# Performance work log

Hardware: AMD Instinct MI355X
Metric: run time of the kernel (lower is better)

## Reference

```python
import jax, jax.numpy as jnp
import numpy as np

B, NGT, G, C = 2, 64, 6, 64
NVOX = 100000            # occupied voxels per batch element
STRIDE = 4               # x_conv3 stride
RADIUS = 0.4             # pool radius (meters)
PCR = (0.0, -40.0, -3.0)
VOX = (0.05, 0.05, 0.1)
DZ, DY, DX = 10, 400, 352  # downsampled sparse grid (z, y, x)


def setup_inputs() -> dict:
    key = jax.random.key(0)
    k = jax.random.split(key, 10)
    cx = jax.random.uniform(k[0], (B, NGT, 1), minval=5.0, maxval=65.0)
    cy = jax.random.uniform(k[1], (B, NGT, 1), minval=-35.0, maxval=35.0)
    cz = jax.random.uniform(k[2], (B, NGT, 1), minval=-1.5, maxval=0.5)
    dims = jax.random.uniform(k[3], (B, NGT, 3), minval=1.5, maxval=4.5)
    heading = jax.random.uniform(k[4], (B, NGT, 1), minval=-np.pi, maxval=np.pi)
    label = jax.random.randint(k[5], (B, NGT, 1), 1, 4).astype(jnp.float32)
    gt_boxes = jnp.concatenate([cx, cy, cz, dims, heading, label], -1)

    def make_voxels(kc, kf):
        kz, ky, kx = jax.random.split(kc, 3)
        z = jax.random.randint(kz, (B * NVOX,), 0, DZ)
        y = jax.random.randint(ky, (B * NVOX,), 0, DY)
        x = jax.random.randint(kx, (B * NVOX,), 0, DX)
        b = jnp.repeat(jnp.arange(B), NVOX)
        coords = jnp.stack([b, z, y, x], 1).astype(jnp.int32)  # (N, 4) bzyx
        feats = jax.random.normal(kf, (B * NVOX, C), dtype=jnp.float32)
        return coords, feats

    cd, fd = make_voxels(k[6], k[7])
    cs, fs = make_voxels(k[8], k[9])
    return {"gt_boxes": gt_boxes,
            "voxel_coords_dir": cd, "voxel_feats_dir": fd,
            "voxel_coords_dsr": cs, "voxel_feats_dsr": fs}


def _grid_points(gt_boxes):
    # get_dense_grid_points + rotate_points_along_z + global shift
    rois = gt_boxes.reshape(-1, gt_boxes.shape[-1])  # (R, 8)
    g = jnp.arange(G, dtype=jnp.float32)
    idx = jnp.stack(jnp.meshgrid(g, g, g, indexing='ij'), -1).reshape(-1, 3)  # (G^3, 3)
    size = rois[:, 3:6]
    local = (idx[None] + 0.5) / G * size[:, None] - size[:, None] * 0.5  # (R, G^3, 3)
    h = rois[:, 6]
    c, s = jnp.cos(h)[:, None], jnp.sin(h)[:, None]
    x, y, z = local[..., 0], local[..., 1], local[..., 2]
    rot = jnp.stack([x * c - y * s, x * s + y * c, z], -1)
    return rot + rois[:, None, 0:3]  # (R, G^3, 3) global grid points


def _pool(grid_xyz, grid_zyx, gbatch, coords, feats):
    # voxel2pinds hash table: (B, DZ, DY, DX) -> point index or -1
    Ntot = coords.shape[0]
    v2p = jnp.full((B, DZ, DY, DX), -1, jnp.int32)
    v2p = v2p.at[coords[:, 0], coords[:, 1], coords[:, 2], coords[:, 3]].set(
        jnp.arange(Ntot, dtype=jnp.int32))
    # voxel centers (get_voxel_centers with downsample=STRIDE)
    vsz = jnp.array([VOX[0] * STRIDE, VOX[1] * STRIDE, VOX[2] * STRIDE], jnp.float32)
    vox_xyz = (coords[:, jnp.array([3, 2, 1])].astype(jnp.float32) + 0.5) * vsz + jnp.array(PCR, jnp.float32)
    # 3x3x3 neighbor window (QUERY_RANGES = [1,1,1])
    o = jnp.arange(-1, 2)
    offs = jnp.stack(jnp.meshgrid(o, o, o, indexing='ij'), -1).reshape(-1, 3)  # (27, 3) zyx
    nb = grid_zyx[:, None, :] + offs[None]  # (M, 27, 3)
    dims = jnp.array([DZ, DY, DX])
    inb = jnp.all((nb >= 0) & (nb < dims), -1)
    nbc = jnp.clip(nb, 0, dims - 1)
    flat = ((gbatch[:, None] * DZ + nbc[..., 0]) * DY + nbc[..., 1]) * DX + nbc[..., 2]
    pidx = v2p.reshape(-1)[flat]  # (M, 27)
    valid = inb & (pidx >= 0)
    psafe = jnp.where(valid, pidx, 0)
    nxyz = vox_xyz[psafe]  # (M, 27, 3)
    d2 = jnp.sum((nxyz - grid_xyz[:, None]) ** 2, -1)
    m = (valid & (d2 < RADIUS * RADIUS)).astype(feats.dtype)  # ball-query mask
    nf = feats[psafe]  # (M, 27, C) irregular gather
    return jnp.einsum('mkc,mk->mc', nf, m) / jnp.maximum(m.sum(-1), 1.0)[:, None]


def _forward(gt_boxes, voxel_coords_dir, voxel_feats_dir, voxel_coords_dsr, voxel_feats_dsr):
    grid = _grid_points(gt_boxes)            # (R, G^3, 3)
    grid_xyz = grid.reshape(-1, 3)           # (M, 3)
    cf = jnp.floor((grid_xyz - jnp.array(PCR, jnp.float32)) / jnp.array(VOX, jnp.float32))
    cds = jnp.floor(cf / STRIDE).astype(jnp.int32)  # xyz coords at stride
    grid_zyx = cds[:, ::-1]
    R = gt_boxes.shape[0] * gt_boxes.shape[1]
    gbatch = jnp.repeat(jnp.arange(B), NGT * G ** 3)

    def branch(coords, feats):
        p = _pool(grid_xyz, grid_zyx, gbatch, coords, feats)  # (M, C)
        gfeat = p.reshape(R, G ** 3, C).mean(1)               # avg_pool1d over grid pts
        n = jnp.sqrt(jnp.sum(gfeat ** 2, -1, keepdims=True))
        return gfeat / jnp.maximum(n, 1e-12)                  # F.normalize(dim=1)

    fdir = branch(voxel_coords_dir, voxel_feats_dir)
    fdsr = branch(voxel_coords_dsr, voxel_feats_dsr)
    return jnp.mean(jnp.abs(jnp.sum(fdir * fdsr, -1)))


def reference(gt_boxes, voxel_coords_dir, voxel_feats_dir, voxel_coords_dsr, voxel_feats_dsr):
    return _forward(gt_boxes, voxel_coords_dir, voxel_feats_dir, voxel_coords_dsr, voxel_feats_dsr)
```

## Files before the change

### kernel.cpp

```cpp
#include <hip/hip_runtime.h>

#define B_     2
#define NGT_   64
#define G_     6
#define C_     64
#define NVOX_  100000
#define DZ_    10
#define DY_    400
#define DX_    352
#define NPTS   (B_ * NVOX_)
#define NROI   (B_ * NGT_)
#define NGP    (G_ * G_ * G_)
#define M_     (NROI * NGP)
#define VCELLS (B_ * DZ_ * DY_ * DX_)

#define WPB    8
#define JPR    (NGP / WPB)
#define SCAT_BLOCKS ((2 * NPTS + 255) / 256)
#define POOL_BLOCKS (2 * M_ / WPB)

__global__ __launch_bounds__(256) void scatter_kernel(
    const int* __restrict__ cdir, const int* __restrict__ cdsr,
    int* __restrict__ v2p) {
  int i = blockIdx.x * 256 + threadIdx.x;
  if (i >= 2 * NPTS) return;
  int br = (i >= NPTS) ? 1 : 0;
  int p  = i - br * NPTS;
  const int* cb = br ? cdsr : cdir;
  int4 v = ((const int4*)cb)[p];
  int flat = ((v.x * DZ_ + v.y) * DY_ + v.z) * DX_ + v.w;
  atomicMax(&v2p[(long long)br * VCELLS + flat], p);
}

__global__ __launch_bounds__(512) void pool_kernel(
    const float* __restrict__ gt,
    const float* __restrict__ fdir, const float* __restrict__ fdsr,
    const int* __restrict__ v2p, float* __restrict__ part) {
#pragma clang fp contract(off)
  __shared__ float red[WPB][C_];
  int wid  = threadIdx.x >> 6;
  int lane = threadIdx.x & 63;
  int w    = blockIdx.x * WPB + wid;
  int br   = (w >= M_) ? 1 : 0;
  int rem  = w - br * M_;
  int roi  = rem / NGP;
  int gp   = rem - roi * NGP;

  const float* fb  = br ? fdsr : fdir;
  const int*   vpb = v2p + (long long)br * VCELLS;

  const float* r8 = gt + roi * 8;
  float cx = r8[0], cy = r8[1], cz = r8[2];
  float d0 = r8[3], d1 = r8[4], d2s = r8[5];
  float h  = r8[6];

  int ii = gp / 36, jj = (gp / 6) % 6, kk = gp % 6;
  float tx = (ii + 0.5f) / 6.0f;
  float ty = (jj + 0.5f) / 6.0f;
  float tz = (kk + 0.5f) / 6.0f;
  float lx = tx * d0 - d0 * 0.5f;
  float ly = ty * d1 - d1 * 0.5f;
  float lz = tz * d2s - d2s * 0.5f;
  float ch = cosf(h), sh = sinf(h);
  float gx = (lx * ch - ly * sh) + cx;
  float gy = (lx * sh + ly * ch) + cy;
  float gz = lz + cz;

  float fx = floorf((gx - 0.0f)   / 0.05f);
  float fy = floorf((gy + 40.0f)  / 0.05f);
  float fz = floorf((gz + 3.0f)   / 0.1f);
  int ixc = (int)floorf(fx * 0.25f);
  int iyc = (int)floorf(fy * 0.25f);
  int izc = (int)floorf(fz * 0.25f);

  int b = roi >> 6;

  int  pidx_l = -1;
  bool valid  = false;
  if (lane < 27) {
    int oz = lane / 9 - 1, oy = (lane / 3) % 3 - 1, ox = lane % 3 - 1;
    int nz = izc + oz, ny = iyc + oy, nx = ixc + ox;
    if (nz >= 0 && nz < DZ_ && ny >= 0 && ny < DY_ && nx >= 0 && nx < DX_) {
      float vx = ((float)nx + 0.5f) * 0.2f + 0.0f;
      float vy = ((float)ny + 0.5f) * 0.2f + (-40.0f);
      float vz = ((float)nz + 0.5f) * 0.4f + (-3.0f);
      float ddx = vx - gx, ddy = vy - gy, ddz = vz - gz;
      float dd = (ddx * ddx + ddy * ddy) + ddz * ddz;
      if (dd < 0.16f) {
        int flat = ((b * DZ_ + nz) * DY_ + ny) * DX_ + nx;
        int p = vpb[flat];
        if (p >= 0) { valid = true; pidx_l = p; }
      }
    }
  }

  unsigned long long ball = __ballot(valid);
  int cnt = __popcll(ball);
  float acc = 0.0f;
  unsigned long long mm = ball;
  while (mm) {
    int k = (int)__builtin_ctzll(mm);
    mm &= mm - 1;
    int p = __shfl(pidx_l, k, 64);
    acc += fb[(long long)p * C_ + lane];
  }
  float pooled = acc / fmaxf((float)cnt, 1.0f);

  red[wid][lane] = pooled;
  __syncthreads();
  if (wid == 0) {
    float s = 0.0f;
#pragma unroll
    for (int q = 0; q < WPB; ++q) s += red[q][lane];
    part[(long long)blockIdx.x * C_ + lane] = s;
  }
}

__global__ __launch_bounds__(64) void reduce_kernel(
    const float* __restrict__ part, float* __restrict__ gsum) {
  int t = threadIdx.x;
  const float* p = part + (long long)blockIdx.x * JPR * C_;
  float s = 0.0f;
#pragma unroll
  for (int j = 0; j < JPR; ++j) s += p[j * C_ + t];
  gsum[blockIdx.x * C_ + t] = s;
}

__global__ __launch_bounds__(1024) void final_kernel(
    const float* __restrict__ gsum, float* __restrict__ out) {
  __shared__ float partsm[16];
  int wave = threadIdx.x >> 6, lane = threadIdx.x & 63;
  float acc = 0.0f;
  for (int r = wave; r < NROI; r += 16) {
    float a = gsum[r * C_ + lane];
    float b = gsum[(NROI + r) * C_ + lane];
    float dot = a * b, na = a * a, nb = b * b;
    for (int off = 32; off; off >>= 1) {
      dot += __shfl_xor(dot, off, 64);
      na  += __shfl_xor(na,  off, 64);
      nb  += __shfl_xor(nb,  off, 64);
    }
    acc += fabsf(dot) / (fmaxf(sqrtf(na), 1e-12f) * fmaxf(sqrtf(nb), 1e-12f));
  }
  if (lane == 0) partsm[wave] = acc;
  __syncthreads();
  if (threadIdx.x == 0) {
    float s = 0.0f;
    for (int i = 0; i < 16; ++i) s += partsm[i];
    out[0] = s / 128.0f;
  }
}

extern "C" void kernel_launch(void* const* d_in, const int* in_sizes, int n_in,
                              void* d_out, int out_size, void* d_ws, size_t ws_size,
                              hipStream_t stream) {
  const float* gt   = (const float*)d_in[0];
  const int*   cdir = (const int*)d_in[1];
  const float* fdir = (const float*)d_in[2];
  const int*   cdsr = (const int*)d_in[3];
  const float* fdsr = (const float*)d_in[4];
  float* out = (float*)d_out;

  int*   v2p  = (int*)d_ws;
  float* part = (float*)((char*)d_ws + (size_t)2 * VCELLS * 4);
  float* gsum = part + (size_t)POOL_BLOCKS * C_;

  scatter_kernel<<<SCAT_BLOCKS, 256, 0, stream>>>(cdir, cdsr, v2p);
  pool_kernel<<<POOL_BLOCKS, 512, 0, stream>>>(gt, fdir, fdsr, v2p, part);
  reduce_kernel<<<256, 64, 0, stream>>>(part, gsum);
  final_kernel<<<1, 1024, 0, stream>>>(gsum, out);
}
```

Measured before the change: 167.9 us.

## Batch four feature gathers per iteration and fuse reduce with final kernel

The pooling loop now extracts up to four neighbor indices before issuing their feature loads, so several independent global loads can be in flight at once instead of one serialized load per iteration. The separate reduce and single-block final kernels are merged into one per-ROI kernel that reduces both branches, computes the normalized dot term and atomically adds it into the output, which is zeroed in the scatter kernel. This removes one kernel launch and the serial single-block tail, at the cost of a non-deterministic float atomic summation order.

```diff
diff --git a/kernel.cpp b/kernel.cpp
--- a/kernel.cpp
+++ b/kernel.cpp
@@ -21,8 +21,9 @@
 
 __global__ __launch_bounds__(256) void scatter_kernel(
     const int* __restrict__ cdir, const int* __restrict__ cdsr,
-    int* __restrict__ v2p) {
+    int* __restrict__ v2p, float* __restrict__ out) {
   int i = blockIdx.x * 256 + threadIdx.x;
+  if (i == 0) out[0] = 0.0f;
   if (i >= 2 * NPTS) return;
   int br = (i >= NPTS) ? 1 : 0;
   int p  = i - br * NPTS;
@@ -99,10 +100,19 @@
   float acc = 0.0f;
   unsigned long long mm = ball;
   while (mm) {
-    int k = (int)__builtin_ctzll(mm);
-    mm &= mm - 1;
-    int p = __shfl(pidx_l, k, 64);
-    acc += fb[(long long)p * C_ + lane];
+    int p0, p1 = -1, p2 = -1, p3 = -1;
+    { int k = (int)__builtin_ctzll(mm); mm &= mm - 1; p0 = __shfl(pidx_l, k, 64); }
+    if (mm) { int k = (int)__builtin_ctzll(mm); mm &= mm - 1; p1 = __shfl(pidx_l, k, 64); }
+    if (mm) { int k = (int)__builtin_ctzll(mm); mm &= mm - 1; p2 = __shfl(pidx_l, k, 64); }
+    if (mm) { int k = (int)__builtin_ctzll(mm); mm &= mm - 1; p3 = __shfl(pidx_l, k, 64); }
+    float v0 = fb[(long long)p0 * C_ + lane];
+    float v1 = (p1 >= 0) ? fb[(long long)p1 * C_ + lane] : 0.0f;
+    float v2 = (p2 >= 0) ? fb[(long long)p2 * C_ + lane] : 0.0f;
+    float v3 = (p3 >= 0) ? fb[(long long)p3 * C_ + lane] : 0.0f;
+    acc += v0;
+    if (p1 >= 0) acc += v1;
+    if (p2 >= 0) acc += v2;
+    if (p3 >= 0) acc += v3;
   }
   float pooled = acc / fmaxf((float)cnt, 1.0f);
 
@@ -116,38 +126,26 @@
   }
 }
 
-__global__ __launch_bounds__(64) void reduce_kernel(
-    const float* __restrict__ part, float* __restrict__ gsum) {
+__global__ __launch_bounds__(64) void reduce_final_kernel(
+    const float* __restrict__ part, float* __restrict__ out) {
   int t = threadIdx.x;
-  const float* p = part + (long long)blockIdx.x * JPR * C_;
-  float s = 0.0f;
+  int r = blockIdx.x;
+  const float* pa = part + (long long)r * JPR * C_;
+  const float* pb = part + (long long)(NROI * JPR + r * JPR) * C_;
+  float a = 0.0f, b = 0.0f;
 #pragma unroll
-  for (int j = 0; j < JPR; ++j) s += p[j * C_ + t];
-  gsum[blockIdx.x * C_ + t] = s;
-}
-
-__global__ __launch_bounds__(1024) void final_kernel(
-    const float* __restrict__ gsum, float* __restrict__ out) {
-  __shared__ float partsm[16];
-  int wave = threadIdx.x >> 6, lane = threadIdx.x & 63;
-  float acc = 0.0f;
-  for (int r = wave; r < NROI; r += 16) {
-    float a = gsum[r * C_ + lane];
-    float b = gsum[(NROI + r) * C_ + lane];
-    float dot = a * b, na = a * a, nb = b * b;
-    for (int off = 32; off; off >>= 1) {
-      dot += __shfl_xor(dot, off, 64);
-      na  += __shfl_xor(na,  off, 64);
-      nb  += __shfl_xor(nb,  off, 64);
-    }
-    acc += fabsf(dot) / (fmaxf(sqrtf(na), 1e-12f) * fmaxf(sqrtf(nb), 1e-12f));
+  for (int j = 0; j < JPR; ++j) a += pa[j * C_ + t];
+#pragma unroll
+  for (int j = 0; j < JPR; ++j) b += pb[j * C_ + t];
+  float dot = a * b, na = a * a, nb = b * b;
+  for (int off = 32; off; off >>= 1) {
+    dot += __shfl_xor(dot, off, 64);
+    na  += __shfl_xor(na,  off, 64);
+    nb  += __shfl_xor(nb,  off, 64);
   }
-  if (lane == 0) partsm[wave] = acc;
-  __syncthreads();
-  if (threadIdx.x == 0) {
-    float s = 0.0f;
-    for (int i = 0; i < 16; ++i) s += partsm[i];
-    out[0] = s / 128.0f;
+  if (t == 0) {
+    float term = fabsf(dot) / (fmaxf(sqrtf(na), 1e-12f) * fmaxf(sqrtf(nb), 1e-12f));
+    atomicAdd(out, term * (1.0f / 128.0f));
   }
 }
 
@@ -163,10 +161,8 @@
 
   int*   v2p  = (int*)d_ws;
   float* part = (float*)((char*)d_ws + (size_t)2 * VCELLS * 4);
-  float* gsum = part + (size_t)POOL_BLOCKS * C_;
 
-  scatter_kernel<<<SCAT_BLOCKS, 256, 0, stream>>>(cdir, cdsr, v2p);
+  scatter_kernel<<<SCAT_BLOCKS, 256, 0, stream>>>(cdir, cdsr, v2p, out);
   pool_kernel<<<POOL_BLOCKS, 512, 0, stream>>>(gt, fdir, fdsr, v2p, part);
-  reduce_kernel<<<256, 64, 0, stream>>>(part, gsum);
-  final_kernel<<<1, 1024, 0, stream>>>(gsum, out);
+  reduce_final_kernel<<<NROI, 64, 0, stream>>>(part, out);
 }
```

After: 160.4 us. -4.5%, faster.
